# Optimization experiments

Measured on AMD Instinct MI355X. Metric: run time of the kernel, lower is better.

The kernel has to match this reference:

```python
import jax, jax.numpy as jnp
import numpy as np

H = 1024          # hidden_size
NH = 16           # num_attention_heads
HD = H // NH      # head_size
EPS = 1e-5


def setup_inputs() -> dict:
    key = jax.random.key(0)
    ks = jax.random.split(key, 5)
    # xavier_uniform bound for Linear(in, out): sqrt(6/(in+out))
    b_qkv = float(np.sqrt(6.0 / (H + 3 * H)))
    b_out = float(np.sqrt(6.0 / (H + H)))
    return {
        "hidden_states": jax.random.normal(ks[0], (2, 2048, H), dtype=jnp.float32),
        "ln_gamma": jnp.ones((H,), jnp.float32),
        "ln_beta": jnp.zeros((H,), jnp.float32),
        "W_qkv": jax.random.uniform(ks[1], (3 * H, H), jnp.float32, -b_qkv, b_qkv),
        "b_qkv": jnp.zeros((3 * H,), jnp.float32),
        "W_out": jax.random.uniform(ks[2], (H, H), jnp.float32, -b_out, b_out),
        "b_out": jnp.zeros((H,), jnp.float32),
    }


def _attn_block(x, ln_gamma, ln_beta, W_qkv, b_qkv, W_out, b_out):
    B, S, _ = x.shape
    # Pre-LN
    mu = jnp.mean(x, axis=-1, keepdims=True)
    var = jnp.mean(jnp.square(x - mu), axis=-1, keepdims=True)
    xn = (x - mu) / jnp.sqrt(var + EPS) * ln_gamma + ln_beta
    # fused QKV projection: [B,S,3H]
    qkv = jnp.einsum("bsh,oh->bso", xn, W_qkv) + b_qkv
    qkv = qkv.reshape(B, S, 3, NH, HD).transpose(2, 0, 3, 1, 4)  # [3,B,NH,S,HD]
    q, k, v = qkv[0], qkv[1], qkv[2]
    scores = jnp.einsum("bhqd,bhkd->bhqk", q, k) / jnp.sqrt(jnp.asarray(HD, x.dtype))
    probs = jax.nn.softmax(scores, axis=-1)
    ctx = jnp.einsum("bhqk,bhkd->bhqd", probs, v)
    ctx = ctx.transpose(0, 2, 1, 3).reshape(B, S, H)
    out = jnp.einsum("bsh,oh->bso", ctx, W_out) + b_out  # dropout: eval mode = identity
    return x + out


def reference(hidden_states, ln_gamma, ln_beta, W_qkv, b_qkv, W_out, b_out):
    return _attn_block(hidden_states, ln_gamma, ln_beta, W_qkv, b_qkv, W_out, b_out)
```

## Files before the change

### kernel.cpp

```cpp
#include <hip/hip_runtime.h>
#include <stdint.h>

typedef unsigned short u16;
typedef __attribute__((ext_vector_type(8))) short bf16x8;
typedef __attribute__((ext_vector_type(4))) float f32x4;
typedef __attribute__((ext_vector_type(4))) unsigned int u32x4;
typedef __attribute__((ext_vector_type(2))) unsigned int u32x2;
typedef __attribute__((ext_vector_type(4))) unsigned short u16x4;

#define QSCALE 0.18033688011112042f

typedef __attribute__((address_space(1))) const void gvoid;
typedef __attribute__((address_space(3))) void svoid;

__device__ __forceinline__ void cp16(const u16* g, u16* l) {
    __builtin_amdgcn_global_load_lds((gvoid*)g, (svoid*)l, 16, 0, 0);
}

__device__ __forceinline__ u16 f2bf(float f) {
    uint32_t u = __float_as_uint(f);
    u += 0x7fff + ((u >> 16) & 1);
    return (u16)(u >> 16);
}

__device__ __forceinline__ uint32_t pack_bf2(float lo, float hi) {
    uint32_t a = __float_as_uint(lo) + 0x8000u;
    uint32_t b = __float_as_uint(hi) + 0x8000u;
    return __builtin_amdgcn_perm(b, a, 0x07060302);
}

__global__ __launch_bounds__(256) void k_pre(const float* __restrict__ X,
                                             const float* __restrict__ gam,
                                             const float* __restrict__ bet,
                                             u16* __restrict__ XN,
                                             const float* __restrict__ Wqkv, u16* __restrict__ Wq,
                                             const float* __restrict__ Wout, u16* __restrict__ Wo) {
    __shared__ float red[8];
    const int bid = blockIdx.x;
    if (bid < 4096) {
        int t = bid;
        const float4* xp = (const float4*)(X + (size_t)t * 1024);
        float4 x = xp[threadIdx.x];
        float s  = x.x + x.y + x.z + x.w;
        float s2 = x.x*x.x + x.y*x.y + x.z*x.z + x.w*x.w;
        #pragma unroll
        for (int off = 1; off < 64; off <<= 1) {
            s  += __shfl_xor(s,  off, 64);
            s2 += __shfl_xor(s2, off, 64);
        }
        int lane = threadIdx.x & 63, w = threadIdx.x >> 6;
        if (lane == 0) { red[w] = s; red[w + 4] = s2; }
        __syncthreads();
        s  = red[0] + red[1] + red[2] + red[3];
        s2 = red[4] + red[5] + red[6] + red[7];
        float mu  = s * (1.0f / 1024.0f);
        float var = s2 * (1.0f / 1024.0f) - mu * mu;
        float rin = rsqrtf(var + 1e-5f);
        float4 g = ((const float4*)gam)[threadIdx.x];
        float4 b = ((const float4*)bet)[threadIdx.x];
        u16x4 o;
        o.x = f2bf((x.x - mu) * rin * g.x + b.x);
        o.y = f2bf((x.y - mu) * rin * g.y + b.y);
        o.z = f2bf((x.z - mu) * rin * g.z + b.z);
        o.w = f2bf((x.w - mu) * rin * g.w + b.w);
        *(u16x4*)(XN + (size_t)t * 1024 + threadIdx.x * 4) = o;
    } else {
        int i = (bid - 4096) * 256 + threadIdx.x;
        const float* src; u16* dst;
        if (i < 786432) { src = Wqkv; dst = Wq; }
        else            { i -= 786432; src = Wout; dst = Wo; }
        float4 v = ((const float4*)src)[i];
        u16x4 o;
        o.x = f2bf(v.x); o.y = f2bf(v.y); o.z = f2bf(v.z); o.w = f2bf(v.w);
        ((u16x4*)dst)[i] = o;
    }
}

__device__ __forceinline__ void gemm_bt_tile(const u16* __restrict__ A, const u16* __restrict__ Bm,
                                             int m0, int n0, u16* As, u16* Bs, f32x4 acc[4][4]) {
    const int tid = threadIdx.x;
    const int lane = tid & 63;
    const int wv = tid >> 6;
    const int qi = lane & 15, g = lane >> 4, swz = qi & 7;
    const int wr = (wv >> 1) * 64, wc = (wv & 1) * 64;
    #pragma unroll
    for (int mi = 0; mi < 4; mi++)
        #pragma unroll
        for (int ni = 0; ni < 4; ni++) acc[mi][ni] = (f32x4){0.f, 0.f, 0.f, 0.f};

    const int row_in = tid >> 3;
    const int cs = (tid & 7) ^ (row_in & 7);
    for (int k0 = 0; k0 < 1024; k0 += 64) {
        __syncthreads();
        #pragma unroll
        for (int i = 0; i < 4; i++) {
            int row = i * 32 + row_in;
            cp16(A  + (size_t)(m0 + row) * 1024 + k0 + cs * 8, As + (i * 256 + wv * 64) * 8);
            cp16(Bm + (size_t)(n0 + row) * 1024 + k0 + cs * 8, Bs + (i * 256 + wv * 64) * 8);
        }
        __syncthreads();
        #pragma unroll
        for (int ks = 0; ks < 2; ks++) {
            bf16x8 af[4], bf[4];
            #pragma unroll
            for (int mi = 0; mi < 4; mi++)
                af[mi] = *(const bf16x8*)(As + (wr + mi * 16 + qi) * 64 + ((ks * 4 + g) ^ swz) * 8);
            #pragma unroll
            for (int ni = 0; ni < 4; ni++)
                bf[ni] = *(const bf16x8*)(Bs + (wc + ni * 16 + qi) * 64 + ((ks * 4 + g) ^ swz) * 8);
            #pragma unroll
            for (int mi = 0; mi < 4; mi++)
                #pragma unroll
                for (int ni = 0; ni < 4; ni++)
                    acc[mi][ni] = __builtin_amdgcn_mfma_f32_16x16x32_bf16(af[mi], bf[ni], acc[mi][ni], 0, 0, 0);
        }
    }
}

__global__ __launch_bounds__(256) void k_qkv(const u16* __restrict__ XN, const u16* __restrict__ Wq,
                                             const float* __restrict__ bqkv,
                                             u16* __restrict__ Q, u16* __restrict__ K,
                                             u16* __restrict__ Vt) {
    __shared__ __align__(16) u16 SMEM[17408];
    u16* As = SMEM;
    u16* Bs = SMEM + 8192;
    f32x4 acc[4][4];
    const int m0 = blockIdx.y * 128, n0 = blockIdx.x * 128;
    gemm_bt_tile(XN, Wq, m0, n0, As, Bs, acc);
    const int lane = threadIdx.x & 63, wid = threadIdx.x >> 6;
    const int g = lane >> 4, qi = lane & 15;
    const int wr = (wid >> 1) * 64, wc = (wid & 1) * 64;
    if (n0 < 2048) {
        const int which = n0 >> 10;
        u16* base = which ? K : Q;
        const float scale = which ? 1.0f : QSCALE;
        #pragma unroll
        for (int mi = 0; mi < 4; mi++)
            #pragma unroll
            for (int ni = 0; ni < 4; ni++)
                #pragma unroll
                for (int i = 0; i < 4; i++) {
                    int m = m0 + wr + mi * 16 + (g * 4 + i);
                    int n = n0 + wc + ni * 16 + qi;
                    float v = (acc[mi][ni][i] + bqkv[n]) * scale;
                    int b = m >> 11, s = m & 2047;
                    int hh = (n >> 6) & 15, d = n & 63;
                    base[((size_t)(b * 16 + hh) * 2048 + s) * 64 + d] = f2bf(v);
                }
    } else {
        __syncthreads();
        u16* Tw = SMEM + wid * 4352;
        #pragma unroll
        for (int mi = 0; mi < 4; mi++)
            #pragma unroll
            for (int ni = 0; ni < 4; ni++) {
                int n = n0 + wc + ni * 16 + qi;
                float bq = bqkv[n];
                u16x4 pk;
                pk.x = f2bf(acc[mi][ni][0] + bq);
                pk.y = f2bf(acc[mi][ni][1] + bq);
                pk.z = f2bf(acc[mi][ni][2] + bq);
                pk.w = f2bf(acc[mi][ni][3] + bq);
                *(u16x4*)(Tw + (ni * 16 + qi) * 68 + mi * 16 + g * 4) = pk;
            }
        const int head = (n0 + wc - 2048) >> 6;
        const int b = m0 >> 11;
        const int s0 = (m0 + wr) & 2047;
        u16* vrow = Vt + (size_t)(b * 16 + head) * 64 * 2048 + s0 + qi * 4;
        #pragma unroll
        for (int dd = 0; dd < 16; dd++) {
            int d = dd * 4 + g;
            u16x4 val = *(const u16x4*)(Tw + d * 68 + qi * 4);
            *(u16x4*)(vrow + (size_t)d * 2048) = val;
        }
    }
}

__global__ __launch_bounds__(512) void k_attn(const u16* __restrict__ Q, const u16* __restrict__ K,
                                              const u16* __restrict__ Vt, u16* __restrict__ CTX) {
    __shared__ __align__(16) u16 Ks[2][64 * 64];
    __shared__ __align__(16) u16 Vs[2][64 * 64];
    __shared__ __align__(16) u16 Ps[8][16 * 64];
    const int id = blockIdx.x;
    const int bh = (id & 7) * 4 + ((id >> 3) & 3);
    const int q0 = (id >> 5) * 128;
    const int lane = threadIdx.x & 63, w = threadIdx.x >> 6;
    const int g = lane >> 4, qi = lane & 15, swz = qi & 7;
    const u16* Qp = Q  + (size_t)bh * (2048 * 64);
    const u16* Kp = K  + (size_t)bh * (2048 * 64);
    const u16* Vp = Vt + (size_t)bh * (64 * 2048);
    u16* Pw = Ps[w];

    const int r0 = w * 8 + (lane >> 3);
    const int cs = (lane & 7) ^ (r0 & 7);
    const u16* kg0 = Kp + (size_t)r0 * 64 + cs * 8;
    const u16* vg0 = Vp + (size_t)r0 * 2048 + cs * 8;

    bf16x8 bq[2];
    {
        const u16* qb = Qp + (size_t)(q0 + w * 16 + qi) * 64 + g * 8;
        bq[0] = *(const bf16x8*)(qb);
        bq[1] = *(const bf16x8*)(qb + 32);
    }
    float lsumA = 0.f, lsumB = 0.f;
    f32x4 od[4];
    #pragma unroll
    for (int nt = 0; nt < 4; nt++) od[nt] = (f32x4){0.f, 0.f, 0.f, 0.f};

    cp16(kg0, Ks[0] + w * 512);
    cp16(vg0, Vs[0] + w * 512);

    #define ATTN_STEP(KT, CKS, CVS, PKS, PVS)                                                    \
    {                                                                                            \
        const int kt_ = (KT);                                                                    \
        __syncthreads();                                                                         \
        if (kt_ < 31) {                                                                          \
            cp16(kg0 + 4096, (PKS) + w * 512);                 \
            cp16(vg0 + 64,   (PVS) + w * 512);            \
        }                                                                                        \
        const u16* ksp = (CKS);                                                                  \
        const u16* vsp = (CVS);                                                                  \
        f32x4 sv[4];                                                                             \
        _Pragma("unroll")                                                                        \
        for (int nt = 0; nt < 4; nt++) sv[nt] = (f32x4){0.f, 0.f, 0.f, 0.f};                     \
        _Pragma("unroll")                                                                        \
        for (int ks = 0; ks < 2; ks++)                                                           \
            _Pragma("unroll")                                                                    \
            for (int nt = 0; nt < 4; nt++) {                                                     \
                bf16x8 ak = *(const bf16x8*)(ksp + (nt * 16 + qi) * 64 + ((ks * 4 + g) ^ swz) * 8); \
                sv[nt] = __builtin_amdgcn_mfma_f32_16x16x32_bf16(ak, bq[ks], sv[nt], 0, 0, 0);   \
            }                                                                                    \
        _Pragma("unroll")                                                                        \
        for (int nt = 0; nt < 2; nt++) {                                                         \
            float e0 = __builtin_amdgcn_exp2f(sv[nt][0]);                                        \
            float e1 = __builtin_amdgcn_exp2f(sv[nt][1]);                                        \
            float e2 = __builtin_amdgcn_exp2f(sv[nt][2]);                                        \
            float e3 = __builtin_amdgcn_exp2f(sv[nt][3]);                                        \
            lsumA += e0 + e1; lsumB += e2 + e3;                                                  \
            u32x2 pk = {pack_bf2(e0, e1), pack_bf2(e2, e3)};                                     \
            *(u32x2*)(Pw + qi * 64 + ((2 * nt + (g >> 1)) ^ swz) * 8 + (g & 1) * 4) = pk;        \
        }                                                                                        \
        {                                                                                        \
            bf16x8 bp = *(const bf16x8*)(Pw + qi * 64 + ((0 * 4 + g) ^ swz) * 8);                \
            _Pragma("unroll")                                                                    \
            for (int nt = 0; nt < 4; nt++) {                                                     \
                bf16x8 av = *(const bf16x8*)(vsp + (nt * 16 + qi) * 64 + ((0 * 4 + g) ^ swz) * 8); \
                od[nt] = __builtin_amdgcn_mfma_f32_16x16x32_bf16(av, bp, od[nt], 0, 0, 0);       \
            }                                                                                    \
        }                                                                                        \
        _Pragma("unroll")                                                                        \
        for (int nt = 2; nt < 4; nt++) {                                                         \
            float e0 = __builtin_amdgcn_exp2f(sv[nt][0]);                                        \
            float e1 = __builtin_amdgcn_exp2f(sv[nt][1]);                                        \
            float e2 = __builtin_amdgcn_exp2f(sv[nt][2]);                                        \
            float e3 = __builtin_amdgcn_exp2f(sv[nt][3]);                                        \
            lsumA += e0 + e1; lsumB += e2 + e3;                                                  \
            u32x2 pk = {pack_bf2(e0, e1), pack_bf2(e2, e3)};                                     \
            *(u32x2*)(Pw + qi * 64 + ((2 * nt + (g >> 1)) ^ swz) * 8 + (g & 1) * 4) = pk;        \
        }                                                                                        \
        {                                                                                        \
            bf16x8 bp = *(const bf16x8*)(Pw + qi * 64 + ((1 * 4 + g) ^ swz) * 8);                \
            _Pragma("unroll")                                                                    \
            for (int nt = 0; nt < 4; nt++) {                                                     \
                bf16x8 av = *(const bf16x8*)(vsp + (nt * 16 + qi) * 64 + ((1 * 4 + g) ^ swz) * 8); \
                od[nt] = __builtin_amdgcn_mfma_f32_16x16x32_bf16(av, bp, od[nt], 0, 0, 0);       \
            }                                                                                    \
        }                                                                                        \
        kg0 += 64 * 64; vg0 += 64;                                                               \
    }

    for (int kt = 0; kt < 32; kt += 2) {
        ATTN_STEP(kt,     Ks[0], Vs[0], Ks[1], Vs[1]);
        ATTN_STEP(kt + 1, Ks[1], Vs[1], Ks[0], Vs[0]);
    }
    #undef ATTN_STEP

    float lsum = lsumA + lsumB;
    lsum += __shfl_xor(lsum, 16, 64);
    lsum += __shfl_xor(lsum, 32, 64);
    float inv = 1.0f / lsum;
    const int b = bh >> 4, hh = bh & 15;
    size_t m = (size_t)b * 2048 + q0 + w * 16 + qi;
    u16* cp = CTX + m * 1024 + hh * 64 + g * 4;
    #pragma unroll
    for (int nt = 0; nt < 4; nt++) {
        u16x4 o;
        o.x = f2bf(od[nt][0] * inv); o.y = f2bf(od[nt][1] * inv);
        o.z = f2bf(od[nt][2] * inv); o.w = f2bf(od[nt][3] * inv);
        *(u16x4*)(cp + nt * 16) = o;
    }
}

__global__ __launch_bounds__(256) void k_out(const u16* __restrict__ CTX, const u16* __restrict__ Wo,
                                             const float* __restrict__ bout, const float* __restrict__ X,
                                             float* __restrict__ OUT) {
    __shared__ __align__(16) u16 As[128 * 64], Bs[128 * 64];
    f32x4 acc[4][4];
    const int m0 = blockIdx.y * 128, n0 = blockIdx.x * 128;
    gemm_bt_tile(CTX, Wo, m0, n0, As, Bs, acc);
    const int lane = threadIdx.x & 63, wid = threadIdx.x >> 6;
    const int wr = (wid >> 1) * 64, wc = (wid & 1) * 64;
    #pragma unroll
    for (int mi = 0; mi < 4; mi++)
        #pragma unroll
        for (int ni = 0; ni < 4; ni++)
            #pragma unroll
            for (int i = 0; i < 4; i++) {
                size_t m = m0 + wr + mi * 16 + ((lane >> 4) * 4 + i);
                int n = n0 + wc + ni * 16 + (lane & 15);
                OUT[m * 1024 + n] = acc[mi][ni][i] + bout[n] + X[m * 1024 + n];
            }
}

extern "C" void kernel_launch(void* const* d_in, const int* in_sizes, int n_in,
                              void* d_out, int out_size, void* d_ws, size_t ws_size,
                              hipStream_t stream) {
    const float* X    = (const float*)d_in[0];
    const float* gam  = (const float*)d_in[1];
    const float* bet  = (const float*)d_in[2];
    const float* Wqkv = (const float*)d_in[3];
    const float* bqkv = (const float*)d_in[4];
    const float* Wout = (const float*)d_in[5];
    const float* bout = (const float*)d_in[6];
    float* OUT = (float*)d_out;

    u16* XN  = (u16*)d_ws;
    u16* Q   = XN  + (size_t)4 * 1024 * 1024;
    u16* K   = Q   + (size_t)4 * 1024 * 1024;
    u16* Vt  = K   + (size_t)4 * 1024 * 1024;
    u16* CTX = Vt  + (size_t)4 * 1024 * 1024;
    u16* Wq  = CTX + (size_t)4 * 1024 * 1024;
    u16* Wo  = Wq  + (size_t)3 * 1024 * 1024;

    k_pre<<<8192, 256, 0, stream>>>(X, gam, bet, XN, Wqkv, Wq, Wout, Wo);
    k_qkv<<<dim3(24, 32), 256, 0, stream>>>(XN, Wq, bqkv, Q, K, Vt);
    k_attn<<<512, 512, 0, stream>>>(Q, K, Vt, CTX);
    k_out<<<dim3(8, 32), 256, 0, stream>>>(CTX, Wo, bout, X, OUT);
}
```

Measured before the change: 198.9 us.

## Process two query fragments per wave in attention to reuse K/V LDS reads

The attention kernel drops from 8 waves of 16 query rows each to 4 waves of 32 query rows each. Each K and V fragment read from LDS now feeds two MFMAs, which halves LDS read traffic per MFMA. Each thread issues twice as many cp16 loads to fill the same 64x64 tiles. The cost is more registers per wave (two score and two output accumulator sets) and fewer waves per block to hide latency.

After: 204.1 us. 2.6% more time.

```diff
diff --git a/kernel.cpp b/kernel.cpp
--- a/kernel.cpp
+++ b/kernel.cpp
@@ -176,11 +176,11 @@
     }
 }
 
-__global__ __launch_bounds__(512) void k_attn(const u16* __restrict__ Q, const u16* __restrict__ K,
+__global__ __launch_bounds__(256) void k_attn(const u16* __restrict__ Q, const u16* __restrict__ K,
                                               const u16* __restrict__ Vt, u16* __restrict__ CTX) {
     __shared__ __align__(16) u16 Ks[2][64 * 64];
     __shared__ __align__(16) u16 Vs[2][64 * 64];
-    __shared__ __align__(16) u16 Ps[8][16 * 64];
+    __shared__ __align__(16) u16 Ps[4][32 * 64];
     const int id = blockIdx.x;
     const int bh = (id & 7) * 4 + ((id >> 3) & 3);
     const int q0 = (id >> 5) * 128;
@@ -191,82 +191,102 @@
     const u16* Vp = Vt + (size_t)bh * (64 * 2048);
     u16* Pw = Ps[w];
 
-    const int r0 = w * 8 + (lane >> 3);
-    const int cs = (lane & 7) ^ (r0 & 7);
+    const int r0 = threadIdx.x >> 3;
+    const int cs = (threadIdx.x & 7) ^ (r0 & 7);
     const u16* kg0 = Kp + (size_t)r0 * 64 + cs * 8;
+    const u16* kg1 = kg0 + 32 * 64;
     const u16* vg0 = Vp + (size_t)r0 * 2048 + cs * 8;
-
-    bf16x8 bq[2];
-    {
-        const u16* qb = Qp + (size_t)(q0 + w * 16 + qi) * 64 + g * 8;
-        bq[0] = *(const bf16x8*)(qb);
-        bq[1] = *(const bf16x8*)(qb + 32);
-    }
-    float lsumA = 0.f, lsumB = 0.f;
-    f32x4 od[4];
-    #pragma unroll
-    for (int nt = 0; nt < 4; nt++) od[nt] = (f32x4){0.f, 0.f, 0.f, 0.f};
+    const u16* vg1 = vg0 + 32 * 2048;
+
+    bf16x8 bq[2][2];
+    #pragma unroll
+    for (int f = 0; f < 2; f++) {
+        const u16* qb = Qp + (size_t)(q0 + w * 32 + f * 16 + qi) * 64 + g * 8;
+        bq[f][0] = *(const bf16x8*)(qb);
+        bq[f][1] = *(const bf16x8*)(qb + 32);
+    }
+    float lsum0 = 0.f, lsum1 = 0.f;
+    f32x4 od[2][4];
+    #pragma unroll
+    for (int f = 0; f < 2; f++)
+        #pragma unroll
+        for (int nt = 0; nt < 4; nt++) od[f][nt] = (f32x4){0.f, 0.f, 0.f, 0.f};
 
     cp16(kg0, Ks[0] + w * 512);
+    cp16(kg1, Ks[0] + 2048 + w * 512);
     cp16(vg0, Vs[0] + w * 512);
+    cp16(vg1, Vs[0] + 2048 + w * 512);
 
     #define ATTN_STEP(KT, CKS, CVS, PKS, PVS)                                                    \
     {                                                                                            \
         const int kt_ = (KT);                                                                    \
         __syncthreads();                                                                         \
         if (kt_ < 31) {                                                                          \
-            cp16(kg0 + 4096, (PKS) + w * 512);                 \
-            cp16(vg0 + 64,   (PVS) + w * 512);            \
+            cp16(kg0 + 4096, (PKS) + w * 512);                                                   \
+            cp16(kg1 + 4096, (PKS) + 2048 + w * 512);                                            \
+            cp16(vg0 + 64,   (PVS) + w * 512);                                                   \
+            cp16(vg1 + 64,   (PVS) + 2048 + w * 512);                                            \
         }                                                                                        \
         const u16* ksp = (CKS);                                                                  \
         const u16* vsp = (CVS);                                                                  \
-        f32x4 sv[4];                                                                             \
+        f32x4 sv[2][4];                                                                          \
         _Pragma("unroll")                                                                        \
-        for (int nt = 0; nt < 4; nt++) sv[nt] = (f32x4){0.f, 0.f, 0.f, 0.f};                     \
+        for (int f = 0; f < 2; f++)                                                              \
+            _Pragma("unroll")                                                                    \
+            for (int nt = 0; nt < 4; nt++) sv[f][nt] = (f32x4){0.f, 0.f, 0.f, 0.f};              \
         _Pragma("unroll")                                                                        \
         for (int ks = 0; ks < 2; ks++)                                                           \
             _Pragma("unroll")                                                                    \
             for (int nt = 0; nt < 4; nt++) {                                                     \
                 bf16x8 ak = *(const bf16x8*)(ksp + (nt * 16 + qi) * 64 + ((ks * 4 + g) ^ swz) * 8); \
-                sv[nt] = __builtin_amdgcn_mfma_f32_16x16x32_bf16(ak, bq[ks], sv[nt], 0, 0, 0);   \
+                sv[0][nt] = __builtin_amdgcn_mfma_f32_16x16x32_bf16(ak, bq[0][ks], sv[0][nt], 0, 0, 0); \
+                sv[1][nt] = __builtin_amdgcn_mfma_f32_16x16x32_bf16(ak, bq[1][ks], sv[1][nt], 0, 0, 0); \
             }                                                                                    \
         _Pragma("unroll")                                                                        \
-        for (int nt = 0; nt < 2; nt++) {                                                         \
-            float e0 = __builtin_amdgcn_exp2f(sv[nt][0]);                                        \
-            float e1 = __builtin_amdgcn_exp2f(sv[nt][1]);                                        \
-            float e2 = __builtin_amdgcn_exp2f(sv[nt][2]);                                        \
-            float e3 = __builtin_amdgcn_exp2f(sv[nt][3]);                                        \
-            lsumA += e0 + e1; lsumB += e2 + e3;                                                  \
-            u32x2 pk = {pack_bf2(e0, e1), pack_bf2(e2, e3)};                                     \
-            *(u32x2*)(Pw + qi * 64 + ((2 * nt + (g >> 1)) ^ swz) * 8 + (g & 1) * 4) = pk;        \
-        }                                                                                        \
+        for (int f = 0; f < 2; f++)                                                              \
+            _Pragma("unroll")                                                                    \
+            for (int nt = 0; nt < 2; nt++) {                                                     \
+                float e0 = __builtin_amdgcn_exp2f(sv[f][nt][0]);                                 \
+                float e1 = __builtin_amdgcn_exp2f(sv[f][nt][1]);                                 \
+                float e2 = __builtin_amdgcn_exp2f(sv[f][nt][2]);                                 \
+                float e3 = __builtin_amdgcn_exp2f(sv[f][nt][3]);                                 \
+                if (f == 0) lsum0 += (e0 + e1) + (e2 + e3); else lsum1 += (e0 + e1) + (e2 + e3); \
+                u32x2 pk = {pack_bf2(e0, e1), pack_bf2(e2, e3)};                                 \
+                *(u32x2*)(Pw + (f * 16 + qi) * 64 + ((2 * nt + (g >> 1)) ^ swz) * 8 + (g & 1) * 4) = pk; \
+            }                                                                                    \
         {                                                                                        \
-            bf16x8 bp = *(const bf16x8*)(Pw + qi * 64 + ((0 * 4 + g) ^ swz) * 8);                \
+            bf16x8 bp0 = *(const bf16x8*)(Pw + qi * 64 + (g ^ swz) * 8);                         \
+            bf16x8 bp1 = *(const bf16x8*)(Pw + (16 + qi) * 64 + (g ^ swz) * 8);                  \
             _Pragma("unroll")                                                                    \
             for (int nt = 0; nt < 4; nt++) {                                                     \
-                bf16x8 av = *(const bf16x8*)(vsp + (nt * 16 + qi) * 64 + ((0 * 4 + g) ^ swz) * 8); \
-                od[nt] = __builtin_amdgcn_mfma_f32_16x16x32_bf16(av, bp, od[nt], 0, 0, 0);       \
+                bf16x8 av = *(const bf16x8*)(vsp + (nt * 16 + qi) * 64 + (g ^ swz) * 8);         \
+                od[0][nt] = __builtin_amdgcn_mfma_f32_16x16x32_bf16(av, bp0, od[0][nt], 0, 0, 0); \
+                od[1][nt] = __builtin_amdgcn_mfma_f32_16x16x32_bf16(av, bp1, od[1][nt], 0, 0, 0); \
             }                                                                                    \
         }                                                                                        \
         _Pragma("unroll")                                                                        \
-        for (int nt = 2; nt < 4; nt++) {                                                         \
-            float e0 = __builtin_amdgcn_exp2f(sv[nt][0]);                                        \
-            float e1 = __builtin_amdgcn_exp2f(sv[nt][1]);                                        \
-            float e2 = __builtin_amdgcn_exp2f(sv[nt][2]);                                        \
-            float e3 = __builtin_amdgcn_exp2f(sv[nt][3]);                                        \
-            lsumA += e0 + e1; lsumB += e2 + e3;                                                  \
-            u32x2 pk = {pack_bf2(e0, e1), pack_bf2(e2, e3)};                                     \
-            *(u32x2*)(Pw + qi * 64 + ((2 * nt + (g >> 1)) ^ swz) * 8 + (g & 1) * 4) = pk;        \
+        for (int f = 0; f < 2; f++)                                                              \
+            _Pragma("unroll")                                                                    \
+            for (int nt = 2; nt < 4; nt++) {                                                     \
+                float e0 = __builtin_amdgcn_exp2f(sv[f][nt][0]);                                 \
+                float e1 = __builtin_amdgcn_exp2f(sv[f][nt][1]);                                 \
+                float e2 = __builtin_amdgcn_exp2f(sv[f][nt][2]);                                 \
+                float e3 = __builtin_amdgcn_exp2f(sv[f][nt][3]);                                 \
+                if (f == 0) lsum0 += (e0 + e1) + (e2 + e3); else lsum1 += (e0 + e1) + (e2 + e3); \
+                u32x2 pk = {pack_bf2(e0, e1), pack_bf2(e2, e3)};                                 \
+                *(u32x2*)(Pw + (f * 16 + qi) * 64 + ((2 * nt + (g >> 1)) ^ swz) * 8 + (g & 1) * 4) = pk; \
+            }                                                                                    \
+        {                                                                                        \
+            bf16x8 bp0 = *(const bf16x8*)(Pw + qi * 64 + ((4 + g) ^ swz) * 8);                   \
+            bf16x8 bp1 = *(const bf16x8*)(Pw + (16 + qi) * 64 + ((4 + g) ^ swz) * 8);            \
+            _Pragma("unroll")                                                                    \
+            for (int nt = 0; nt < 4; nt++) {                                                     \
+                bf16x8 av = *(const bf16x8*)(vsp + (nt * 16 + qi) * 64 + ((4 + g) ^ swz) * 8);   \
+                od[0][nt] = __builtin_amdgcn_mfma_f32_16x16x32_bf16(av, bp0, od[0][nt], 0, 0, 0); \
+                od[1][nt] = __builtin_amdgcn_mfma_f32_16x16x32_bf16(av, bp1, od[1][nt], 0, 0, 0); \
+            }                                                                                    \
         }                                                                                        \
-        {                                                                                        \
-            bf16x8 bp = *(const bf16x8*)(Pw + qi * 64 + ((1 * 4 + g) ^ swz) * 8);                \
-            _Pragma("unroll")                                                                    \
-            for (int nt = 0; nt < 4; nt++) {                                                     \
-                bf16x8 av = *(const bf16x8*)(vsp + (nt * 16 + qi) * 64 + ((1 * 4 + g) ^ swz) * 8); \
-                od[nt] = __builtin_amdgcn_mfma_f32_16x16x32_bf16(av, bp, od[nt], 0, 0, 0);       \
-            }                                                                                    \
-        }                                                                                        \
-        kg0 += 64 * 64; vg0 += 64;                                                               \
+        kg0 += 4096; kg1 += 4096; vg0 += 64; vg1 += 64;                                          \
     }
 
     for (int kt = 0; kt < 32; kt += 2) {
@@ -275,19 +295,23 @@
     }
     #undef ATTN_STEP
 
-    float lsum = lsumA + lsumB;
-    lsum += __shfl_xor(lsum, 16, 64);
-    lsum += __shfl_xor(lsum, 32, 64);
-    float inv = 1.0f / lsum;
+    lsum0 += __shfl_xor(lsum0, 16, 64);
+    lsum0 += __shfl_xor(lsum0, 32, 64);
+    lsum1 += __shfl_xor(lsum1, 16, 64);
+    lsum1 += __shfl_xor(lsum1, 32, 64);
+    const float inv[2] = {1.0f / lsum0, 1.0f / lsum1};
     const int b = bh >> 4, hh = bh & 15;
-    size_t m = (size_t)b * 2048 + q0 + w * 16 + qi;
-    u16* cp = CTX + m * 1024 + hh * 64 + g * 4;
-    #pragma unroll
-    for (int nt = 0; nt < 4; nt++) {
-        u16x4 o;
-        o.x = f2bf(od[nt][0] * inv); o.y = f2bf(od[nt][1] * inv);
-        o.z = f2bf(od[nt][2] * inv); o.w = f2bf(od[nt][3] * inv);
-        *(u16x4*)(cp + nt * 16) = o;
+    #pragma unroll
+    for (int f = 0; f < 2; f++) {
+        size_t m = (size_t)b * 2048 + q0 + w * 32 + f * 16 + qi;
+        u16* cp = CTX + m * 1024 + hh * 64 + g * 4;
+        #pragma unroll
+        for (int nt = 0; nt < 4; nt++) {
+            u16x4 o;
+            o.x = f2bf(od[f][nt][0] * inv[f]); o.y = f2bf(od[f][nt][1] * inv[f]);
+            o.z = f2bf(od[f][nt][2] * inv[f]); o.w = f2bf(od[f][nt][3] * inv[f]);
+            *(u16x4*)(cp + nt * 16) = o;
+        }
     }
 }
 
@@ -334,6 +358,6 @@
 
     k_pre<<<8192, 256, 0, stream>>>(X, gam, bet, XN, Wqkv, Wq, Wout, Wo);
     k_qkv<<<dim3(24, 32), 256, 0, stream>>>(XN, Wq, bqkv, Q, K, Vt);
-    k_attn<<<512, 512, 0, stream>>>(Q, K, Vt, CTX);
+    k_attn<<<512, 256, 0, stream>>>(Q, K, Vt, CTX);
     k_out<<<dim3(8, 32), 256, 0, stream>>>(CTX, Wo, bout, X, OUT);
 }
```
